# Kernel tuning notes

Measured on AMD Instinct MI355X. Metric: run time of the kernel, lower is better.

## Reference

```python
import jax, jax.numpy as jnp
import numpy as np

NUM_CLASSES = 100
NUM_PROTOS = 10
FEAT_DIM = 1024
BATCH = 16384
NALL = NUM_CLASSES * NUM_PROTOS


def setup_inputs() -> dict:
    key = jax.random.key(0)
    k1, k2, k3 = jax.random.split(key, 3)
    x = jax.random.normal(k1, (BATCH, FEAT_DIM), dtype=jnp.float32)
    protos = jax.random.normal(k2, (NALL, FEAT_DIM), dtype=jnp.float32)
    enc_w = jax.random.normal(k3, (FEAT_DIM, FEAT_DIM), dtype=jnp.float32) / np.sqrt(FEAT_DIM)
    enc_b = jnp.zeros((FEAT_DIM,), dtype=jnp.float32)
    return {"x": x, "protos": protos, "enc_w": enc_w, "enc_b": enc_b}


def reference(x, protos, enc_w, enc_b):
    # encoder(protos): linear projection, (nall, F)
    ep = protos @ enc_w + enc_b
    # Pairwise euclidean distance via GEMM-based squared-distance trick:
    x_sq = jnp.sum(x * x, axis=-1, keepdims=True)            # (B, 1)
    p_sq = jnp.sum(ep * ep, axis=-1)                          # (nall,)
    d2 = x_sq - 2.0 * (x @ ep.T) + p_sq[None, :]              # (B, nall)
    d = jnp.sqrt(jnp.maximum(d2, 0.0))                        # L2 norm, clamp fp error
    # reshape matches torch: index = proto * num_classes + class
    d = d.reshape(x.shape[0], NUM_PROTOS, NUM_CLASSES)
    return jnp.min(d, axis=1)                                 # (B, num_classes)
```

## Files before the change

kernel.cpp:

```cpp
#include <hip/hip_runtime.h>
#include <hip/hip_bf16.h>
#include <stdint.h>

#define FEAT 1024
#define NALL 1000
#define NPAD 1120
#define NCLS 100

typedef __attribute__((ext_vector_type(8))) short short8;
typedef __attribute__((ext_vector_type(4))) float f32x4;
typedef __attribute__((ext_vector_type(4))) unsigned short us4;

__device__ __forceinline__ unsigned short f2bf(float f) {
    union { float f; uint32_t u; } v; v.f = f;
    uint32_t u = v.u;
    return (unsigned short)((u + 0x7FFFu + ((u >> 16) & 1u)) >> 16);
}

__device__ __forceinline__ void gload16(const void* g, void* l) {
    __builtin_amdgcn_global_load_lds((__attribute__((address_space(1))) void*)g,
                                     (__attribute__((address_space(3))) void*)l,
                                     16, 0, 0);
}

__global__ __launch_bounds__(256) void k_prep_x(const float* __restrict__ x,
                                                unsigned short* __restrict__ xb,
                                                float* __restrict__ xsq) {
    int row = blockIdx.x * 4 + (threadIdx.x >> 6);
    int lane = threadIdx.x & 63;
    const float4* xr = (const float4*)(x + (size_t)row * FEAT);
    float s = 0.f;
#pragma unroll
    for (int i = 0; i < 4; ++i) {
        float4 v = xr[lane + i * 64];
        s += v.x * v.x + v.y * v.y + v.z * v.z + v.w * v.w;
        us4 o;
        o[0] = f2bf(v.x); o[1] = f2bf(v.y); o[2] = f2bf(v.z); o[3] = f2bf(v.w);
        *(us4*)(xb + (size_t)row * FEAT + (size_t)(lane + i * 64) * 4) = o;
    }
#pragma unroll
    for (int off = 32; off; off >>= 1) s += __shfl_xor(s, off);
    if (lane == 0) xsq[row] = s;
}

__global__ __launch_bounds__(256) void k_prep_protos(const float* __restrict__ p,
                                                     unsigned short* __restrict__ pb) {
    int row = blockIdx.x;
    int t = threadIdx.x;
    us4 o;
    if (row < NALL) {
        float4 v = ((const float4*)(p + (size_t)row * FEAT))[t];
        o[0] = f2bf(v.x); o[1] = f2bf(v.y); o[2] = f2bf(v.z); o[3] = f2bf(v.w);
    } else {
        o[0] = 0; o[1] = 0; o[2] = 0; o[3] = 0;
    }
    *(us4*)(pb + (size_t)row * FEAT + (size_t)t * 4) = o;
}

__global__ __launch_bounds__(256) void k_transpose_w(const float* __restrict__ w,
                                                     unsigned short* __restrict__ wt) {
    __shared__ float tile[32][33];
    int bx = blockIdx.x, by = blockIdx.y;
    int tx = threadIdx.x & 31, ty = threadIdx.x >> 5;
#pragma unroll
    for (int i = 0; i < 4; ++i) {
        int r = by * 32 + ty + i * 8;
        tile[ty + i * 8][tx] = w[(size_t)r * FEAT + bx * 32 + tx];
    }
    __syncthreads();
#pragma unroll
    for (int i = 0; i < 4; ++i) {
        int r = bx * 32 + ty + i * 8;
        wt[(size_t)r * FEAT + by * 32 + tx] = f2bf(tile[tx][ty + i * 8]);
    }
}

__global__ __launch_bounds__(256) void k_enc_gemm(const unsigned short* __restrict__ A,
                                                  const unsigned short* __restrict__ B,
                                                  const float* __restrict__ bias,
                                                  unsigned short* __restrict__ epb) {
    __shared__ __align__(16) char smem[32768];
    int bm0 = (blockIdx.x >> 3) * 128;
    int bn0 = (blockIdx.x & 7) * 128;
    int tid = threadIdx.x, lane = tid & 63, wid = tid >> 6;
    int wm = wid >> 1, wn = wid & 1;
    int ls = lane >> 4, lf = lane & 15;
    f32x4 acc[4][4] = {};
    for (int k0 = 0; k0 < FEAT; k0 += 64) {
        __syncthreads();
#pragma unroll
        for (int i = 0; i < 4; ++i) {
            int ci = wid + i * 4;
            int r = ci * 8 + (lane >> 3), c = (lane & 7) * 8;
            gload16(A + (size_t)(bm0 + r) * FEAT + k0 + c, smem + ci * 1024);
            gload16(B + (size_t)(bn0 + r) * FEAT + k0 + c, smem + 16384 + ci * 1024);
        }
        __syncthreads();
#pragma unroll
        for (int kk = 0; kk < 64; kk += 32) {
            short8 a[4], b[4];
#pragma unroll
            for (int f = 0; f < 4; ++f) {
                a[f] = *(const short8*)(smem + (wm * 64 + f * 16 + lf) * 128 + (kk + ls * 8) * 2);
                b[f] = *(const short8*)(smem + 16384 + (wn * 64 + f * 16 + lf) * 128 + (kk + ls * 8) * 2);
            }
#pragma unroll
            for (int fm = 0; fm < 4; ++fm)
#pragma unroll
                for (int fn = 0; fn < 4; ++fn)
                    acc[fm][fn] = __builtin_amdgcn_mfma_f32_16x16x32_bf16(a[fm], b[fn], acc[fm][fn], 0, 0, 0);
        }
    }
    int tr = ls * 4, tc = lf;
#pragma unroll
    for (int fn = 0; fn < 4; ++fn) {
        int col = bn0 + wn * 64 + fn * 16 + tc;
        float bb = bias[col];
#pragma unroll
        for (int fm = 0; fm < 4; ++fm) {
#pragma unroll
            for (int r = 0; r < 4; ++r) {
                int row = bm0 + wm * 64 + fm * 16 + tr + r;
                if (row < NALL) {
                    int pr = (row % 100) * 10 + row / 100;
                    epb[(size_t)pr * FEAT + col] = f2bf(acc[fm][fn][r] + bb);
                }
            }
        }
    }
}

__global__ __launch_bounds__(256) void k_psq(const unsigned short* __restrict__ epb,
                                             float* __restrict__ psq) {
    int row = blockIdx.x * 4 + (threadIdx.x >> 6);
    int lane = threadIdx.x & 63;
    if (row >= NPAD) return;
    float s = 0.f;
    const short8* r8 = (const short8*)(epb + (size_t)row * FEAT);
#pragma unroll
    for (int i = 0; i < 2; ++i) {
        short8 v = r8[lane + i * 64];
#pragma unroll
        for (int j = 0; j < 8; ++j) {
            union { uint32_t u; float f; } c;
            c.u = ((uint32_t)(unsigned short)v[j]) << 16;
            s += c.f * c.f;
        }
    }
#pragma unroll
    for (int off = 32; off; off >>= 1) s += __shfl_xor(s, off);
    if (lane == 0) psq[row] = (row < NALL) ? s : 1e30f;
}

__global__ __launch_bounds__(256) void k_main(const unsigned short* __restrict__ xb,
                                              const unsigned short* __restrict__ epb,
                                              const float* __restrict__ xsq,
                                              const float* __restrict__ psq,
                                              float* __restrict__ out) {
    __shared__ __align__(16) char smem[74880];
    const int bid = blockIdx.x;
    const int swz = (bid & 7) * 112 + (bid >> 3);
    const int bm0 = (swz / 7) * 128;
    const int bn0 = (swz % 7) * 160;
    const int tid = threadIdx.x, lane = tid & 63, wid = tid >> 6;
    const int wm = wid >> 1, wn = wid & 1;
    const int ls = lane >> 4, lf = lane & 15;
    float* xsq_s = (float*)(smem + 73728);
    float* psq_s = (float*)(smem + 74240);
    if (tid < 128) xsq_s[tid] = xsq[bm0 + tid];
    if (tid < 160) psq_s[tid] = psq[bn0 + tid];

    const int sr = lane >> 3, scb = lane & 7;
    const int scol = ((scb ^ sr) << 3);
    const unsigned short* aptr[4];
    const unsigned short* bptr[5];
#pragma unroll
    for (int i = 0; i < 4; ++i)
        aptr[i] = xb + (size_t)(bm0 + (wid + i * 4) * 8 + sr) * FEAT + scol;
#pragma unroll
    for (int i = 0; i < 5; ++i)
        bptr[i] = epb + (size_t)(bn0 + (wid + i * 4) * 8 + sr) * FEAT + scol;

    int raA[4], raB[5];
#pragma unroll
    for (int f = 0; f < 4; ++f) raA[f] = (wm * 64 + f * 16 + lf) * 128;
#pragma unroll
    for (int f = 0; f < 5; ++f) raB[f] = 16384 + (wn * 80 + f * 16 + lf) * 128;
    const int sw = lf & 7;

    f32x4 acc[4][5] = {};

#define STAGE(T, CUR) do {                                                     \
    char* lb_ = smem + (CUR) * 36864;                                          \
    _Pragma("unroll")                                                          \
    for (int i_ = 0; i_ < 4; ++i_)                                             \
        gload16(aptr[i_] + (T) * 64, lb_ + (wid + i_ * 4) * 1024);             \
    _Pragma("unroll")                                                          \
    for (int i_ = 0; i_ < 5; ++i_)                                             \
        gload16(bptr[i_] + (T) * 64, lb_ + 16384 + (wid + i_ * 4) * 1024);     \
} while (0)

    STAGE(0, 0);
    __syncthreads();
#pragma unroll
    for (int t = 0; t < 16; ++t) {
        const int cur = t & 1;
        if (t < 15) STAGE(t + 1, cur ^ 1);
        const char* base = (const char*)smem + cur * 36864;
#pragma unroll
        for (int kk2 = 0; kk2 < 2; ++kk2) {
            const int off = (((kk2 * 4 + ls) ^ sw) << 4);
            short8 a[4], b[5];
#pragma unroll
            for (int f = 0; f < 4; ++f)
                a[f] = *(const short8*)(base + raA[f] + off);
#pragma unroll
            for (int f = 0; f < 5; ++f)
                b[f] = *(const short8*)(base + raB[f] + off);
#pragma unroll
            for (int fm = 0; fm < 4; ++fm)
#pragma unroll
                for (int fn = 0; fn < 5; ++fn)
                    acc[fm][fn] = __builtin_amdgcn_mfma_f32_16x16x32_bf16(a[fm], b[fn], acc[fm][fn], 0, 0, 0);
        }
        __syncthreads();
    }
#undef STAGE

    float* dls = (float*)smem;
    const int tr = ls * 4, tc = lf;
    const int cls0 = bn0 / 10;
#pragma unroll
    for (int p = 0; p < 2; ++p) {
        __syncthreads();
#pragma unroll
        for (int f2 = 0; f2 < 2; ++f2) {
            int fm = p * 2 + f2;
#pragma unroll
            for (int fn = 0; fn < 5; ++fn) {
                int col = wn * 80 + fn * 16 + tc;
                float pq = psq_s[col];
#pragma unroll
                for (int r = 0; r < 4; ++r) {
                    float d2 = xsq_s[wm * 64 + fm * 16 + tr + r] - 2.f * acc[fm][fn][r] + pq;
                    dls[(wm * 32 + f2 * 16 + tr + r) * 161 + col] = sqrtf(fmaxf(d2, 0.f));
                }
            }
        }
        __syncthreads();
#pragma unroll
        for (int tI = 0; tI < 4; ++tI) {
            int task = tid + tI * 256;
            int rr = task >> 4, cl = task & 15;
            float m = 1e30f;
#pragma unroll
            for (int j = 0; j < 10; ++j) m = fminf(m, dls[rr * 161 + cl * 10 + j]);
            int grow = bm0 + (rr >> 5) * 64 + p * 32 + (rr & 31);
            int gcls = cls0 + cl;
            if (gcls < NCLS) out[(size_t)grow * NCLS + gcls] = m;
        }
    }
}

extern "C" void kernel_launch(void* const* d_in, const int* in_sizes, int n_in,
                              void* d_out, int out_size, void* d_ws, size_t ws_size,
                              hipStream_t stream) {
    const float* x      = (const float*)d_in[0];
    const float* protos = (const float*)d_in[1];
    const float* enc_w  = (const float*)d_in[2];
    const float* enc_b  = (const float*)d_in[3];
    float* out = (float*)d_out;
    char* ws = (char*)d_ws;

    unsigned short* xb  = (unsigned short*)ws;
    unsigned short* epb = (unsigned short*)(ws + 33554432);
    unsigned short* prb = (unsigned short*)(ws + 35848192);
    unsigned short* wtb = (unsigned short*)(ws + 37945344);
    float* xsq = (float*)(ws + 40042496);
    float* psq = (float*)(ws + 40108032);

    hipMemsetAsync(epb + (size_t)1000 * FEAT, 0, (size_t)120 * FEAT * 2, stream);

    k_prep_x<<<4096, 256, 0, stream>>>(x, xb, xsq);
    k_prep_protos<<<1024, 256, 0, stream>>>(protos, prb);
    k_transpose_w<<<dim3(32, 32), 256, 0, stream>>>(enc_w, wtb);
    k_enc_gemm<<<64, 256, 0, stream>>>(prb, wtb, enc_b, epb);
    k_psq<<<280, 256, 0, stream>>>(epb, psq);
    k_main<<<896, 256, 0, stream>>>(xb, epb, xsq, psq, out);
}
```

Baseline: 109.8 us.

## Drop LDS double buffering and split epilogue to raise occupancy

Replaces the double-buffered global-to-LDS staging with a single buffer that is filled and consumed between two barriers each K-step. The distance epilogue now runs in four 16-row passes so its scratch fits in the smaller buffer. Together these roughly halve the shared memory per block, so more blocks can be resident per CU. The aim is to hide load latency across blocks instead of inside one block. In exchange, each block loses its own load/compute overlap and pays an extra barrier per iteration, and the K loop is no longer force-unrolled.

```diff
diff --git a/kernel.cpp b/kernel.cpp
--- a/kernel.cpp
+++ b/kernel.cpp
@@ -157,7 +157,7 @@
                                               const float* __restrict__ xsq,
                                               const float* __restrict__ psq,
                                               float* __restrict__ out) {
-    __shared__ __align__(16) char smem[74880];
+    __shared__ __align__(16) char smem[38016];
     const int bid = blockIdx.x;
     const int swz = (bid & 7) * 112 + (bid >> 3);
     const int bm0 = (swz / 7) * 128;
@@ -165,8 +165,8 @@
     const int tid = threadIdx.x, lane = tid & 63, wid = tid >> 6;
     const int wm = wid >> 1, wn = wid & 1;
     const int ls = lane >> 4, lf = lane & 15;
-    float* xsq_s = (float*)(smem + 73728);
-    float* psq_s = (float*)(smem + 74240);
+    float* xsq_s = (float*)(smem + 36864);
+    float* psq_s = (float*)(smem + 37376);
     if (tid < 128) xsq_s[tid] = xsq[bm0 + tid];
     if (tid < 160) psq_s[tid] = psq[bn0 + tid];
 
@@ -190,72 +190,62 @@
 
     f32x4 acc[4][5] = {};
 
-#define STAGE(T, CUR) do {                                                     \
-    char* lb_ = smem + (CUR) * 36864;                                          \
-    _Pragma("unroll")                                                          \
-    for (int i_ = 0; i_ < 4; ++i_)                                             \
-        gload16(aptr[i_] + (T) * 64, lb_ + (wid + i_ * 4) * 1024);             \
-    _Pragma("unroll")                                                          \
-    for (int i_ = 0; i_ < 5; ++i_)                                             \
-        gload16(bptr[i_] + (T) * 64, lb_ + 16384 + (wid + i_ * 4) * 1024);     \
-} while (0)
-
-    STAGE(0, 0);
-    __syncthreads();
-#pragma unroll
     for (int t = 0; t < 16; ++t) {
-        const int cur = t & 1;
-        if (t < 15) STAGE(t + 1, cur ^ 1);
-        const char* base = (const char*)smem + cur * 36864;
+        __syncthreads();
+#pragma unroll
+        for (int i = 0; i < 4; ++i)
+            gload16(aptr[i], smem + (wid + i * 4) * 1024);
+#pragma unroll
+        for (int i = 0; i < 5; ++i)
+            gload16(bptr[i], smem + 16384 + (wid + i * 4) * 1024);
+#pragma unroll
+        for (int i = 0; i < 4; ++i) aptr[i] += 64;
+#pragma unroll
+        for (int i = 0; i < 5; ++i) bptr[i] += 64;
+        __syncthreads();
 #pragma unroll
         for (int kk2 = 0; kk2 < 2; ++kk2) {
             const int off = (((kk2 * 4 + ls) ^ sw) << 4);
             short8 a[4], b[5];
 #pragma unroll
             for (int f = 0; f < 4; ++f)
-                a[f] = *(const short8*)(base + raA[f] + off);
+                a[f] = *(const short8*)(smem + raA[f] + off);
 #pragma unroll
             for (int f = 0; f < 5; ++f)
-                b[f] = *(const short8*)(base + raB[f] + off);
+                b[f] = *(const short8*)(smem + raB[f] + off);
 #pragma unroll
             for (int fm = 0; fm < 4; ++fm)
 #pragma unroll
                 for (int fn = 0; fn < 5; ++fn)
                     acc[fm][fn] = __builtin_amdgcn_mfma_f32_16x16x32_bf16(a[fm], b[fn], acc[fm][fn], 0, 0, 0);
         }
-        __syncthreads();
-    }
-#undef STAGE
+    }
 
     float* dls = (float*)smem;
     const int tr = ls * 4, tc = lf;
     const int cls0 = bn0 / 10;
 #pragma unroll
-    for (int p = 0; p < 2; ++p) {
-        __syncthreads();
-#pragma unroll
-        for (int f2 = 0; f2 < 2; ++f2) {
-            int fm = p * 2 + f2;
-#pragma unroll
-            for (int fn = 0; fn < 5; ++fn) {
-                int col = wn * 80 + fn * 16 + tc;
-                float pq = psq_s[col];
-#pragma unroll
-                for (int r = 0; r < 4; ++r) {
-                    float d2 = xsq_s[wm * 64 + fm * 16 + tr + r] - 2.f * acc[fm][fn][r] + pq;
-                    dls[(wm * 32 + f2 * 16 + tr + r) * 161 + col] = sqrtf(fmaxf(d2, 0.f));
-                }
+    for (int p = 0; p < 4; ++p) {
+        __syncthreads();
+#pragma unroll
+        for (int fn = 0; fn < 5; ++fn) {
+            int col = wn * 80 + fn * 16 + tc;
+            float pq = psq_s[col];
+#pragma unroll
+            for (int r = 0; r < 4; ++r) {
+                float d2 = xsq_s[wm * 64 + p * 16 + tr + r] - 2.f * acc[p][fn][r] + pq;
+                dls[(wm * 16 + tr + r) * 161 + col] = sqrtf(fmaxf(d2, 0.f));
             }
         }
         __syncthreads();
 #pragma unroll
-        for (int tI = 0; tI < 4; ++tI) {
-            int task = tid + tI * 256;
+        for (int i = 0; i < 2; ++i) {
+            int task = tid + i * 256;
             int rr = task >> 4, cl = task & 15;
             float m = 1e30f;
 #pragma unroll
             for (int j = 0; j < 10; ++j) m = fminf(m, dls[rr * 161 + cl * 10 + j]);
-            int grow = bm0 + (rr >> 5) * 64 + p * 32 + (rr & 31);
+            int grow = bm0 + (rr >> 4) * 64 + p * 16 + (rr & 15);
             int gcls = cls0 + cl;
             if (gcls < NCLS) out[(size_t)grow * NCLS + gcls] = m;
         }
```

After: 119.4 us. +8.7%, slower.
